# Performance work log

Hardware: AMD Instinct MI355X
Metric: run time of the kernel (lower is better)

Reference implementation:

```python
import jax, jax.numpy as jnp
import numpy as np

B, D = 8192, 4096  # batch, flattened feature dim
RATIO = 0.2


def setup_inputs() -> dict:
    key = jax.random.key(0)
    x = jax.random.normal(key, (B, D), dtype=jnp.float32)
    k = int(np.ceil(RATIO * D))  # 820, static for lax.top_k
    return {"x": x, "k": k}


def reference(x, k):
    # k-Winners-Take-All: per row, keep values >= k-th largest, zero the rest.
    kth_largest = jax.lax.top_k(x, k)[0][:, -1]  # [B]
    return jnp.where(x < kth_largest[:, None], 0.0, x)
```

## Files before the change

### kernel.cpp

```cpp
#include <hip/hip_runtime.h>
#include <stdint.h>

#define D_DIM   4096
#define THREADS 256
#define NBINS   4096

__global__ __launch_bounds__(THREADS, 8)
void kwta_kernel(const float* __restrict__ x, const int* __restrict__ kptr,
                 float* __restrict__ out) {
    __shared__ uint32_t hist[NBINS];
    __shared__ uint32_t wtot[4];
    __shared__ int pub_bin, pub_kp, ns;

    const int t    = threadIdx.x;
    const int wid  = t >> 6;
    const int lane = t & 63;
    const int row  = blockIdx.x;
    const size_t base = (size_t)row * D_DIM;
    const float4* __restrict__ xr = reinterpret_cast<const float4*>(x + base);
    float4* __restrict__ orow     = reinterpret_cast<float4*>(out + base);
    const int k = kptr[0];

    uint32_t u[16];
    #pragma unroll
    for (int j = 0; j < 4; ++j) {
        float4 v = xr[t + j * THREADS];
        uint32_t b[4] = { __float_as_uint(v.x), __float_as_uint(v.y),
                          __float_as_uint(v.z), __float_as_uint(v.w) };
        #pragma unroll
        for (int e = 0; e < 4; ++e) {
            uint32_t f = b[e];
            u[j * 4 + e] = ((int32_t)f < 0) ? ~f : (f | 0x80000000u);
        }
    }

    #pragma unroll
    for (int j = 0; j < 4; ++j)
        reinterpret_cast<uint4*>(hist)[t + j * THREADS] = make_uint4(0, 0, 0, 0);
    if (t == 0) ns = 0;
    __syncthreads();

    #pragma unroll
    for (int e = 0; e < 16; ++e)
        atomicAdd(&hist[u[e] >> 20], 1u);
    __syncthreads();

    uint32_t h[16];
    #pragma unroll
    for (int j = 0; j < 4; ++j) {
        uint4 hv = reinterpret_cast<const uint4*>(hist)[4 * t + j];
        h[4 * j + 0] = hv.x; h[4 * j + 1] = hv.y;
        h[4 * j + 2] = hv.z; h[4 * j + 3] = hv.w;
    }
    uint32_t T = 0;
    #pragma unroll
    for (int i = 0; i < 16; ++i) T += h[i];
    uint32_t W = T;
    #pragma unroll
    for (int m = 1; m <= 32; m <<= 1) {
        uint32_t o = (uint32_t)__shfl_down((int)W, m, 64);
        if (lane + m < 64) W += o;
    }
    if (lane == 0) wtot[wid] = W;
    __syncthreads();
    uint32_t above = W - T;
    #pragma unroll
    for (int w = 0; w < 4; ++w)
        if (w > wid) above += wtot[w];
    if (above < (uint32_t)k && (uint32_t)k <= above + T) {
        uint32_t cum = above;
        #pragma unroll
        for (int i = 15; i >= 0; --i) {
            cum += h[i];
            if (cum >= (uint32_t)k) {
                pub_bin = 16 * t + i;
                pub_kp  = k - (int)(cum - h[i]);
                break;
            }
        }
    }
    __syncthreads();
    const uint32_t bin = (uint32_t)pub_bin;
    const int kp = pub_kp;

    #pragma unroll
    for (int e = 0; e < 16; ++e) {
        const bool m = (u[e] >> 20) == bin;
        unsigned long long mk = __ballot(m);
        int cnt = (int)__popcll(mk);
        int bs = 0;
        if (lane == 0 && cnt) bs = atomicAdd(&ns, cnt);
        bs = __shfl(bs, 0, 64);
        if (m) {
            int pos = bs + (int)__popcll(mk & ((1ull << lane) - 1ull));
            hist[pos] = u[e];
        }
    }
    __syncthreads();
    const int N = ns;

    uint32_t lo = 0, hi = 0xFFFFFu;
    if (N <= 256) {
        uint32_t v[4];
        #pragma unroll
        for (int c = 0; c < 4; ++c) {
            int idx = 64 * c + lane;
            v[c] = (idx < N) ? (hist[idx] & 0xFFFFFu) : 0u;
        }
        #pragma unroll 1
        while (lo < hi) {
            uint32_t mid = lo + ((hi - lo + 1u) >> 1);
            int c = 0;
            #pragma unroll
            for (int j = 0; j < 4; ++j)
                c += (int)__popcll(__ballot(v[j] >= mid));
            if (c >= kp) lo = mid; else hi = mid - 1u;
        }
    } else {
        #pragma unroll 1
        while (lo < hi) {
            uint32_t mid = lo + ((hi - lo + 1u) >> 1);
            int c = 0;
            for (int cb = 0; cb < N; cb += 64) {
                uint32_t vv = 0;
                if (cb + lane < N) vv = hist[cb + lane] & 0xFFFFFu;
                c += (int)__popcll(__ballot(vv >= mid));
            }
            if (c >= kp) lo = mid; else hi = mid - 1u;
        }
    }
    const uint32_t thr = (bin << 20) | lo;

    #pragma unroll
    for (int j = 0; j < 4; ++j) {
        float4 o;
        float* po = &o.x;
        #pragma unroll
        for (int e = 0; e < 4; ++e) {
            uint32_t uu = u[j * 4 + e];
            uint32_t f  = (uu & 0x80000000u) ? (uu ^ 0x80000000u) : ~uu;
            po[e] = (uu >= thr) ? __uint_as_float(f) : 0.0f;
        }
        orow[t + j * THREADS] = o;
    }
}

extern "C" void kernel_launch(void* const* d_in, const int* in_sizes, int n_in,
                              void* d_out, int out_size, void* d_ws, size_t ws_size,
                              hipStream_t stream) {
    const float* x    = (const float*)d_in[0];
    const int*   kptr = (const int*)d_in[1];
    float*       out  = (float*)d_out;
    const int rows = out_size / D_DIM;
    kwta_kernel<<<rows, THREADS, 0, stream>>>(x, kptr, out);
}
```

Baseline: 232.0 us.

## Process two rows per block with 2048-bin histograms and warp-level compaction

Each 256-thread block now handles two rows, with two waves per row and 32 elements per thread. The first-pass histogram shrinks to 2048 bins (11 bits) per row, so both row histograms fit in the same shared buffer. Only one wave per row scans its histogram, which drops the cross-wave total and one barrier. Candidate compaction now does one atomic per wave instead of one per element group. The trade-off is more registers per thread (occupancy hint lowered to 6), more candidates per coarser bin, and a longer second-pass binary search over 21 bits.

```diff
diff --git a/kernel.cpp b/kernel.cpp
--- a/kernel.cpp
+++ b/kernel.cpp
@@ -3,28 +3,30 @@
 
 #define D_DIM   4096
 #define THREADS 256
-#define NBINS   4096
+#define NBINS   2048
+#define ROWS    2
 
-__global__ __launch_bounds__(THREADS, 8)
+__global__ __launch_bounds__(THREADS, 6)
 void kwta_kernel(const float* __restrict__ x, const int* __restrict__ kptr,
                  float* __restrict__ out) {
-    __shared__ uint32_t hist[NBINS];
-    __shared__ uint32_t wtot[4];
-    __shared__ int pub_bin, pub_kp, ns;
+    __shared__ uint32_t hist[2 * NBINS];
+    __shared__ int pub_bin[2], pub_kp[2], ns[2];
 
     const int t    = threadIdx.x;
+    const int lane = t & 63;
     const int wid  = t >> 6;
-    const int lane = t & 63;
-    const int row  = blockIdx.x;
+    const int r    = wid >> 1;
+    const int wip  = wid & 1;
+    const int row  = blockIdx.x * ROWS + r;
     const size_t base = (size_t)row * D_DIM;
     const float4* __restrict__ xr = reinterpret_cast<const float4*>(x + base);
     float4* __restrict__ orow     = reinterpret_cast<float4*>(out + base);
-    const int k = kptr[0];
+    const uint32_t uk = (uint32_t)kptr[0];
 
-    uint32_t u[16];
+    uint32_t u[32];
     #pragma unroll
-    for (int j = 0; j < 4; ++j) {
-        float4 v = xr[t + j * THREADS];
+    for (int j = 0; j < 8; ++j) {
+        float4 v = xr[wip * 512 + j * 64 + lane];
         uint32_t b[4] = { __float_as_uint(v.x), __float_as_uint(v.y),
                           __float_as_uint(v.z), __float_as_uint(v.w) };
         #pragma unroll
@@ -37,75 +39,93 @@
     #pragma unroll
     for (int j = 0; j < 4; ++j)
         reinterpret_cast<uint4*>(hist)[t + j * THREADS] = make_uint4(0, 0, 0, 0);
-    if (t == 0) ns = 0;
+    if (t < 2) ns[t] = 0;
     __syncthreads();
 
+    uint32_t* __restrict__ h = &hist[r * NBINS];
     #pragma unroll
-    for (int e = 0; e < 16; ++e)
-        atomicAdd(&hist[u[e] >> 20], 1u);
+    for (int e = 0; e < 32; ++e)
+        atomicAdd(&h[u[e] >> 21], 1u);
     __syncthreads();
 
-    uint32_t h[16];
-    #pragma unroll
-    for (int j = 0; j < 4; ++j) {
-        uint4 hv = reinterpret_cast<const uint4*>(hist)[4 * t + j];
-        h[4 * j + 0] = hv.x; h[4 * j + 1] = hv.y;
-        h[4 * j + 2] = hv.z; h[4 * j + 3] = hv.w;
-    }
-    uint32_t T = 0;
-    #pragma unroll
-    for (int i = 0; i < 16; ++i) T += h[i];
-    uint32_t W = T;
-    #pragma unroll
-    for (int m = 1; m <= 32; m <<= 1) {
-        uint32_t o = (uint32_t)__shfl_down((int)W, m, 64);
-        if (lane + m < 64) W += o;
-    }
-    if (lane == 0) wtot[wid] = W;
-    __syncthreads();
-    uint32_t above = W - T;
-    #pragma unroll
-    for (int w = 0; w < 4; ++w)
-        if (w > wid) above += wtot[w];
-    if (above < (uint32_t)k && (uint32_t)k <= above + T) {
-        uint32_t cum = above;
+    if (wip == 0) {
+        const uint4* __restrict__ h4 = reinterpret_cast<const uint4*>(h);
+        uint32_t g[8];
+        uint32_t T = 0;
         #pragma unroll
-        for (int i = 15; i >= 0; --i) {
-            cum += h[i];
-            if (cum >= (uint32_t)k) {
-                pub_bin = 16 * t + i;
-                pub_kp  = k - (int)(cum - h[i]);
-                break;
+        for (int j = 0; j < 8; ++j) {
+            uint4 hv = h4[lane * 8 + j];
+            g[j] = hv.x + hv.y + hv.z + hv.w;
+            T += g[j];
+        }
+        uint32_t W = T;
+        #pragma unroll
+        for (int m = 1; m <= 32; m <<= 1) {
+            uint32_t o = (uint32_t)__shfl_down((int)W, m, 64);
+            if (lane + m < 64) W += o;
+        }
+        const uint32_t above = W - T;
+        if (above < uk && uk <= above + T) {
+            uint32_t cum = above;
+            int jg = 0; bool fj = false;
+            #pragma unroll
+            for (int j = 7; j >= 0; --j) {
+                if (!fj) {
+                    if (cum + g[j] >= uk) { jg = j; fj = true; }
+                    else cum += g[j];
+                }
             }
+            uint4 hv = h4[lane * 8 + jg];
+            uint32_t c4[4] = { hv.x, hv.y, hv.z, hv.w };
+            int be = 0; bool fe = false;
+            #pragma unroll
+            for (int e = 3; e >= 0; --e) {
+                if (!fe) {
+                    if (cum + c4[e] >= uk) { be = e; fe = true; }
+                    else cum += c4[e];
+                }
+            }
+            pub_bin[r] = lane * 32 + jg * 4 + be;
+            pub_kp[r]  = (int)(uk - cum);
         }
     }
     __syncthreads();
-    const uint32_t bin = (uint32_t)pub_bin;
-    const int kp = pub_kp;
 
+    const uint32_t bin = (uint32_t)pub_bin[r];
+    const int      kp  = pub_kp[r];
+
+    const unsigned long long lt = (1ull << lane) - 1ull;
+    int cnt = 0;
     #pragma unroll
-    for (int e = 0; e < 16; ++e) {
-        const bool m = (u[e] >> 20) == bin;
+    for (int e = 0; e < 32; ++e) {
+        unsigned long long mk = __ballot((u[e] >> 21) == bin);
+        cnt += (int)__popcll(mk);
+    }
+    int wbase = 0;
+    if (lane == 0) wbase = atomicAdd(&ns[r], cnt);
+    wbase = __builtin_amdgcn_readfirstlane(wbase);
+    int run = wbase;
+    #pragma unroll
+    for (int e = 0; e < 32; ++e) {
+        const bool m = (u[e] >> 21) == bin;
         unsigned long long mk = __ballot(m);
-        int cnt = (int)__popcll(mk);
-        int bs = 0;
-        if (lane == 0 && cnt) bs = atomicAdd(&ns, cnt);
-        bs = __shfl(bs, 0, 64);
         if (m) {
-            int pos = bs + (int)__popcll(mk & ((1ull << lane) - 1ull));
-            hist[pos] = u[e];
+            int pos = run + (int)__popcll(mk & lt);
+            hist[r == 0 ? pos : 4095 - pos] = u[e];
         }
+        run += (int)__popcll(mk);
     }
     __syncthreads();
-    const int N = ns;
+    const int N = ns[r];
 
-    uint32_t lo = 0, hi = 0xFFFFFu;
+    uint32_t lo = 0, hi = 0x1FFFFFu;
     if (N <= 256) {
         uint32_t v[4];
         #pragma unroll
         for (int c = 0; c < 4; ++c) {
             int idx = 64 * c + lane;
-            v[c] = (idx < N) ? (hist[idx] & 0xFFFFFu) : 0u;
+            uint32_t sv = hist[r == 0 ? idx : 4095 - idx];
+            v[c] = (idx < N) ? (sv & 0x1FFFFFu) : 0u;
         }
         #pragma unroll 1
         while (lo < hi) {
@@ -123,16 +143,17 @@
             int c = 0;
             for (int cb = 0; cb < N; cb += 64) {
                 uint32_t vv = 0;
-                if (cb + lane < N) vv = hist[cb + lane] & 0xFFFFFu;
+                int idx = cb + lane;
+                if (idx < N) vv = hist[r == 0 ? idx : 4095 - idx] & 0x1FFFFFu;
                 c += (int)__popcll(__ballot(vv >= mid));
             }
             if (c >= kp) lo = mid; else hi = mid - 1u;
         }
     }
-    const uint32_t thr = (bin << 20) | lo;
+    const uint32_t thr = (bin << 21) | lo;
 
     #pragma unroll
-    for (int j = 0; j < 4; ++j) {
+    for (int j = 0; j < 8; ++j) {
         float4 o;
         float* po = &o.x;
         #pragma unroll
@@ -141,7 +162,7 @@
             uint32_t f  = (uu & 0x80000000u) ? (uu ^ 0x80000000u) : ~uu;
             po[e] = (uu >= thr) ? __uint_as_float(f) : 0.0f;
         }
-        orow[t + j * THREADS] = o;
+        orow[wip * 512 + j * 64 + lane] = o;
     }
 }
 
@@ -151,6 +172,7 @@
     const float* x    = (const float*)d_in[0];
     const int*   kptr = (const int*)d_in[1];
     float*       out  = (float*)d_out;
-    const int rows = out_size / D_DIM;
-    kwta_kernel<<<rows, THREADS, 0, stream>>>(x, kptr, out);
+    const int rows   = out_size / D_DIM;
+    const int blocks = rows / ROWS;
+    kwta_kernel<<<blocks, THREADS, 0, stream>>>(x, kptr, out);
 }
```

Result: slower. 258.2 us (+11.3%).

## Process four rows per block with next-row prefetch and lighter LDS barriers

Applied to the files above, without the earlier changes.

Each block now handles four consecutive rows and issues the global loads for the next row before working on the current one, so load latency overlaps the histogram and select phases. __syncthreads is replaced by a custom barrier that waits only on LDS counters. The bin search first scans per-uint4 group sums before rereading one group. Candidate compaction uses one LDS atomic per wave instead of one per element. The grid shrinks fourfold (2048 blocks), which lowers parallelism, and rows not divisible by four would be dropped.

```diff
diff --git a/kernel.cpp b/kernel.cpp
--- a/kernel.cpp
+++ b/kernel.cpp
@@ -4,6 +4,13 @@
 #define D_DIM   4096
 #define THREADS 256
 #define NBINS   4096
+#define RPB     4
+
+__device__ __forceinline__ void bar_lds() {
+    asm volatile("s_waitcnt lgkmcnt(0)" ::: "memory");
+    __builtin_amdgcn_s_barrier();
+    asm volatile("" ::: "memory");
+}
 
 __global__ __launch_bounds__(THREADS, 8)
 void kwta_kernel(const float* __restrict__ x, const int* __restrict__ kptr,
@@ -15,133 +22,164 @@
     const int t    = threadIdx.x;
     const int wid  = t >> 6;
     const int lane = t & 63;
-    const int row  = blockIdx.x;
-    const size_t base = (size_t)row * D_DIM;
-    const float4* __restrict__ xr = reinterpret_cast<const float4*>(x + base);
-    float4* __restrict__ orow     = reinterpret_cast<float4*>(out + base);
-    const int k = kptr[0];
+    const uint32_t uk = (uint32_t)kptr[0];
+    const size_t base0 = (size_t)blockIdx.x * RPB * D_DIM;
 
-    uint32_t u[16];
-    #pragma unroll
-    for (int j = 0; j < 4; ++j) {
-        float4 v = xr[t + j * THREADS];
-        uint32_t b[4] = { __float_as_uint(v.x), __float_as_uint(v.y),
-                          __float_as_uint(v.z), __float_as_uint(v.w) };
+    float4 nv[4];
+    {
+        const float4* __restrict__ xr = reinterpret_cast<const float4*>(x + base0);
         #pragma unroll
-        for (int e = 0; e < 4; ++e) {
-            uint32_t f = b[e];
-            u[j * 4 + e] = ((int32_t)f < 0) ? ~f : (f | 0x80000000u);
-        }
+        for (int j = 0; j < 4; ++j) nv[j] = xr[t + j * THREADS];
     }
 
-    #pragma unroll
-    for (int j = 0; j < 4; ++j)
-        reinterpret_cast<uint4*>(hist)[t + j * THREADS] = make_uint4(0, 0, 0, 0);
-    if (t == 0) ns = 0;
-    __syncthreads();
+    #pragma unroll 1
+    for (int g = 0; g < RPB; ++g) {
+        const size_t base = base0 + (size_t)g * D_DIM;
 
-    #pragma unroll
-    for (int e = 0; e < 16; ++e)
-        atomicAdd(&hist[u[e] >> 20], 1u);
-    __syncthreads();
-
-    uint32_t h[16];
-    #pragma unroll
-    for (int j = 0; j < 4; ++j) {
-        uint4 hv = reinterpret_cast<const uint4*>(hist)[4 * t + j];
-        h[4 * j + 0] = hv.x; h[4 * j + 1] = hv.y;
-        h[4 * j + 2] = hv.z; h[4 * j + 3] = hv.w;
-    }
-    uint32_t T = 0;
-    #pragma unroll
-    for (int i = 0; i < 16; ++i) T += h[i];
-    uint32_t W = T;
-    #pragma unroll
-    for (int m = 1; m <= 32; m <<= 1) {
-        uint32_t o = (uint32_t)__shfl_down((int)W, m, 64);
-        if (lane + m < 64) W += o;
-    }
-    if (lane == 0) wtot[wid] = W;
-    __syncthreads();
-    uint32_t above = W - T;
-    #pragma unroll
-    for (int w = 0; w < 4; ++w)
-        if (w > wid) above += wtot[w];
-    if (above < (uint32_t)k && (uint32_t)k <= above + T) {
-        uint32_t cum = above;
+        uint32_t u[16];
         #pragma unroll
-        for (int i = 15; i >= 0; --i) {
-            cum += h[i];
-            if (cum >= (uint32_t)k) {
-                pub_bin = 16 * t + i;
-                pub_kp  = k - (int)(cum - h[i]);
-                break;
+        for (int j = 0; j < 4; ++j) {
+            uint32_t b[4] = { __float_as_uint(nv[j].x), __float_as_uint(nv[j].y),
+                              __float_as_uint(nv[j].z), __float_as_uint(nv[j].w) };
+            #pragma unroll
+            for (int e = 0; e < 4; ++e) {
+                uint32_t f = b[e];
+                u[j * 4 + e] = ((int32_t)f < 0) ? ~f : (f | 0x80000000u);
             }
         }
-    }
-    __syncthreads();
-    const uint32_t bin = (uint32_t)pub_bin;
-    const int kp = pub_kp;
+        if (g + 1 < RPB) {
+            const float4* __restrict__ xr =
+                reinterpret_cast<const float4*>(x + base + D_DIM);
+            #pragma unroll
+            for (int j = 0; j < 4; ++j) nv[j] = xr[t + j * THREADS];
+        }
 
-    #pragma unroll
-    for (int e = 0; e < 16; ++e) {
-        const bool m = (u[e] >> 20) == bin;
-        unsigned long long mk = __ballot(m);
-        int cnt = (int)__popcll(mk);
-        int bs = 0;
-        if (lane == 0 && cnt) bs = atomicAdd(&ns, cnt);
-        bs = __shfl(bs, 0, 64);
-        if (m) {
-            int pos = bs + (int)__popcll(mk & ((1ull << lane) - 1ull));
-            hist[pos] = u[e];
+        #pragma unroll
+        for (int j = 0; j < 4; ++j)
+            reinterpret_cast<uint4*>(hist)[t + j * THREADS] = make_uint4(0, 0, 0, 0);
+        if (t == 0) ns = 0;
+        bar_lds();
+
+        #pragma unroll
+        for (int e = 0; e < 16; ++e)
+            atomicAdd(&hist[u[e] >> 20], 1u);
+        bar_lds();
+
+        uint32_t g4[4]; uint32_t T = 0;
+        #pragma unroll
+        for (int j = 0; j < 4; ++j) {
+            uint4 hv = reinterpret_cast<const uint4*>(hist)[4 * t + j];
+            g4[j] = hv.x + hv.y + hv.z + hv.w;
+            T += g4[j];
         }
-    }
-    __syncthreads();
-    const int N = ns;
+        uint32_t W = T;
+        #pragma unroll
+        for (int m = 1; m <= 32; m <<= 1) {
+            uint32_t o = (uint32_t)__shfl_down((int)W, m, 64);
+            if (lane + m < 64) W += o;
+        }
+        if (lane == 0) wtot[wid] = W;
+        bar_lds();
+        uint32_t above = W - T;
+        #pragma unroll
+        for (int w = 0; w < 4; ++w)
+            if (w > wid) above += wtot[w];
+        if (above < uk && uk <= above + T) {
+            uint32_t cum = above;
+            int jg = 0; bool fj = false;
+            #pragma unroll
+            for (int j = 3; j >= 0; --j) {
+                if (!fj) {
+                    if (cum + g4[j] >= uk) { jg = j; fj = true; }
+                    else cum += g4[j];
+                }
+            }
+            uint4 hv = reinterpret_cast<const uint4*>(hist)[4 * t + jg];
+            uint32_t c4[4] = { hv.x, hv.y, hv.z, hv.w };
+            int be = 0; bool fe = false;
+            #pragma unroll
+            for (int e = 3; e >= 0; --e) {
+                if (!fe) {
+                    if (cum + c4[e] >= uk) { be = e; fe = true; }
+                    else cum += c4[e];
+                }
+            }
+            pub_bin = 16 * t + 4 * jg + be;
+            pub_kp  = (int)(uk - cum);
+        }
+        bar_lds();
+        const uint32_t bin = (uint32_t)pub_bin;
+        const int kp = pub_kp;
 
-    uint32_t lo = 0, hi = 0xFFFFFu;
-    if (N <= 256) {
-        uint32_t v[4];
+        const unsigned long long lt = (1ull << lane) - 1ull;
+        uint32_t mm = 0; int cnt = 0;
         #pragma unroll
-        for (int c = 0; c < 4; ++c) {
-            int idx = 64 * c + lane;
-            v[c] = (idx < N) ? (hist[idx] & 0xFFFFFu) : 0u;
+        for (int e = 0; e < 16; ++e) {
+            const bool m = (u[e] >> 20) == bin;
+            unsigned long long mk = __ballot(m);
+            cnt += (int)__popcll(mk);
+            if (m) mm |= (1u << e);
         }
-        #pragma unroll 1
-        while (lo < hi) {
-            uint32_t mid = lo + ((hi - lo + 1u) >> 1);
-            int c = 0;
+        int wbase = 0;
+        if (lane == 0) wbase = atomicAdd(&ns, cnt);
+        wbase = __builtin_amdgcn_readfirstlane(wbase);
+        int run = wbase;
+        #pragma unroll
+        for (int e = 0; e < 16; ++e) {
+            const bool m = (mm >> e) & 1u;
+            unsigned long long mk = __ballot(m);
+            if (m) hist[run + (int)__popcll(mk & lt)] = u[e];
+            run += (int)__popcll(mk);
+        }
+        bar_lds();
+        const int N = ns;
+
+        uint32_t lo = 0, hi = 0xFFFFFu;
+        if (N <= 256) {
+            uint32_t v[4];
             #pragma unroll
-            for (int j = 0; j < 4; ++j)
-                c += (int)__popcll(__ballot(v[j] >= mid));
-            if (c >= kp) lo = mid; else hi = mid - 1u;
+            for (int c = 0; c < 4; ++c) {
+                int idx = 64 * c + lane;
+                v[c] = (idx < N) ? (hist[idx] & 0xFFFFFu) : 0u;
+            }
+            #pragma unroll 1
+            while (lo < hi) {
+                uint32_t mid = lo + ((hi - lo + 1u) >> 1);
+                int c = 0;
+                #pragma unroll
+                for (int j = 0; j < 4; ++j)
+                    c += (int)__popcll(__ballot(v[j] >= mid));
+                if (c >= kp) lo = mid; else hi = mid - 1u;
+            }
+        } else {
+            #pragma unroll 1
+            while (lo < hi) {
+                uint32_t mid = lo + ((hi - lo + 1u) >> 1);
+                int c = 0;
+                for (int cb = 0; cb < N; cb += 64) {
+                    uint32_t vv = 0;
+                    if (cb + lane < N) vv = hist[cb + lane] & 0xFFFFFu;
+                    c += (int)__popcll(__ballot(vv >= mid));
+                }
+                if (c >= kp) lo = mid; else hi = mid - 1u;
+            }
         }
-    } else {
-        #pragma unroll 1
-        while (lo < hi) {
-            uint32_t mid = lo + ((hi - lo + 1u) >> 1);
-            int c = 0;
-            for (int cb = 0; cb < N; cb += 64) {
-                uint32_t vv = 0;
-                if (cb + lane < N) vv = hist[cb + lane] & 0xFFFFFu;
-                c += (int)__popcll(__ballot(vv >= mid));
+        const uint32_t thr = (bin << 20) | lo;
+
+        float4* __restrict__ orow = reinterpret_cast<float4*>(out + base);
+        #pragma unroll
+        for (int j = 0; j < 4; ++j) {
+            float4 o;
+            float* po = &o.x;
+            #pragma unroll
+            for (int e = 0; e < 4; ++e) {
+                uint32_t uu = u[j * 4 + e];
+                uint32_t f  = (uu & 0x80000000u) ? (uu ^ 0x80000000u) : ~uu;
+                po[e] = (uu >= thr) ? __uint_as_float(f) : 0.0f;
             }
-            if (c >= kp) lo = mid; else hi = mid - 1u;
+            orow[t + j * THREADS] = o;
         }
-    }
-    const uint32_t thr = (bin << 20) | lo;
-
-    #pragma unroll
-    for (int j = 0; j < 4; ++j) {
-        float4 o;
-        float* po = &o.x;
-        #pragma unroll
-        for (int e = 0; e < 4; ++e) {
-            uint32_t uu = u[j * 4 + e];
-            uint32_t f  = (uu & 0x80000000u) ? (uu ^ 0x80000000u) : ~uu;
-            po[e] = (uu >= thr) ? __uint_as_float(f) : 0.0f;
-        }
-        orow[t + j * THREADS] = o;
+        if (g + 1 < RPB) bar_lds();
     }
 }
 
@@ -151,6 +189,7 @@
     const float* x    = (const float*)d_in[0];
     const int*   kptr = (const int*)d_in[1];
     float*       out  = (float*)d_out;
-    const int rows = out_size / D_DIM;
-    kwta_kernel<<<rows, THREADS, 0, stream>>>(x, kptr, out);
+    const int rows   = out_size / D_DIM;
+    const int blocks = rows / RPB;
+    kwta_kernel<<<blocks, THREADS, 0, stream>>>(x, kptr, out);
 }
```

After: 293.6 us. 1.27x slower.
